# Performance work log

Measured on AMD Instinct MI355X. Metric: run time of the kernel, lower is better.

## Reference

```python
import jax, jax.numpy as jnp
import numpy as np

H = 64
N_LAYERS = 3
SIZES = {"atom": 100_000, "bond": 200_000, "motif": 50_000, "cell": 5_000}
# (src_type, dst_type) per relation, in HeteroConv dict order
RELS = [("atom", "atom"), ("atom", "bond"), ("atom", "motif"),
        ("bond", "bond"), ("bond", "motif"), ("motif", "motif"),
        ("atom", "cell"), ("bond", "cell"), ("motif", "cell")]
EDGE_NAMES = ["ei_aa", "ei_ab", "ei_am", "ei_bb", "ei_bm", "ei_mm", "ei_ac", "ei_bc", "ei_mc"]
N_EDGES = [800_000, 400_000, 200_000, 400_000, 200_000, 100_000, 100_000, 200_000, 50_000]


def setup_inputs() -> dict:
    key = jax.random.key(0)
    ks = iter(jax.random.split(key, 64))
    inp = {}
    for t in ["atom", "bond", "motif", "cell"]:
        inp["x_" + t] = jax.random.normal(next(ks), (SIZES[t], H), jnp.float32)
    scale = 1.0 / np.sqrt(H)
    inp["Wl"] = jax.random.normal(next(ks), (N_LAYERS, 9, H, H), jnp.float32) * scale
    inp["bl"] = jax.random.normal(next(ks), (N_LAYERS, 9, H), jnp.float32) * 0.01
    inp["Wr"] = jax.random.normal(next(ks), (N_LAYERS, 9, H, H), jnp.float32) * scale
    inp["proj_W"] = jax.random.normal(next(ks), (H, H), jnp.float32) * scale
    inp["proj_b"] = jax.random.normal(next(ks), (H,), jnp.float32) * 0.01
    inp["out_W"] = jax.random.normal(next(ks), (H, 1), jnp.float32) * scale
    inp["out_b"] = jax.random.normal(next(ks), (1,), jnp.float32) * 0.01
    for name, (st, dt), e in zip(EDGE_NAMES, RELS, N_EDGES):
        src = jax.random.randint(next(ks), (e,), 0, SIZES[st], dtype=jnp.int32)
        dst = jax.random.randint(next(ks), (e,), 0, SIZES[dt], dtype=jnp.int32)
        inp[name] = jnp.stack([src, dst]).astype(jnp.int64)
    return inp


def _sage(x_src, x_dst, ei, Wl_r, bl_r, Wr_r):
    """PyG SAGEConv: lin_l(mean of neighbor src feats) + bias + lin_r(x_dst)."""
    src, dst = ei[0], ei[1]
    n_dst = x_dst.shape[0]
    s = jax.ops.segment_sum(x_src[src], dst, num_segments=n_dst)        # [n_dst, H]
    cnt = jax.ops.segment_sum(jnp.ones_like(dst, dtype=x_src.dtype), dst, num_segments=n_dst)
    agg = s / jnp.maximum(cnt, 1.0)[:, None]                            # mean; 0 for isolated
    return agg @ Wl_r + bl_r + x_dst @ Wr_r


def reference(x_atom, x_bond, x_motif, x_cell, Wl, bl, Wr, proj_W, proj_b,
              out_W, out_b, ei_aa, ei_ab, ei_am, ei_bb, ei_bm, ei_mm,
              ei_ac, ei_bc, ei_mc):
    eis = [ei_aa, ei_ab, ei_am, ei_bb, ei_bm, ei_mm, ei_ac, ei_bc, ei_mc]
    x = {"atom": x_atom, "bond": x_bond, "motif": x_motif, "cell": x_cell}
    for l in range(N_LAYERS):
        acc = {t: jnp.zeros((SIZES[t], H), x_atom.dtype) for t in SIZES}
        for r, (st, dt) in enumerate(RELS):
            acc[dt] = acc[dt] + _sage(x[st], x[dt], eis[r], Wl[l, r], bl[l, r], Wr[l, r])
        x = {t: jax.nn.relu(acc[t]) for t in SIZES}  # HeteroConv aggr='sum' then relu
    h = jax.nn.softplus(x["cell"] @ proj_W + proj_b)
    return h @ out_W + out_b  # [n_cell, 1]
```

## Files before the change

### kernel.cpp

```cpp
#include <hip/hip_runtime.h>
#include <hip/hip_bf16.h>

#define H64 64

typedef __bf16 bf16_t;
typedef __bf16 bf16x8 __attribute__((ext_vector_type(8)));
typedef float f32x4 __attribute__((ext_vector_type(4)));

__device__ __forceinline__ float wload(const void* p, long i, bool f32) {
    return f32 ? ((const float*)p)[i]
               : __bfloat162float(((const __hip_bfloat16*)p)[i]);
}
__device__ __forceinline__ float blo(unsigned v) { return __uint_as_float(v << 16); }
__device__ __forceinline__ float bhi(unsigned v) { return __uint_as_float(v & 0xffff0000u); }
__device__ __forceinline__ unsigned packbf(float lo, float hi) {
    __hip_bfloat162 t;
    t.x = __float2bfloat16(lo);
    t.y = __float2bfloat16(hi);
    return *(unsigned*)&t;
}
__device__ __forceinline__ void acc8(float* s, uint4 v, unsigned m) {
    s[0] += blo(v.x & m); s[1] += bhi(v.x & m);
    s[2] += blo(v.y & m); s[3] += bhi(v.y & m);
    s[4] += blo(v.z & m); s[5] += bhi(v.z & m);
    s[6] += blo(v.w & m); s[7] += bhi(v.w & m);
}

__global__ void detect_k(const unsigned int* __restrict__ eiw, int nwords,
                         const unsigned short* __restrict__ xw,
                         const unsigned short* __restrict__ ww,
                         unsigned int* __restrict__ flags) {
    int t = threadIdx.x;
    unsigned int acc = 0;
    for (int i = 1 + 2 * t; i < nwords; i += 512) acc |= eiw[i];
    if (acc) atomicOr(&flags[0], acc);
    unsigned int cx = 0, cw = 0;
    for (int i = t; i < 8192; i += 256) {
        unsigned short w = xw[i];
        unsigned int e = (w >> 7) & 0xFF;
        if ((w & 0x7FFF) && (e == 0xFF || e < 0x40)) cx++;
        w = ww[i];
        e = (w >> 7) & 0xFF;
        if ((w & 0x7FFF) && (e == 0xFF || e < 0x40)) cw++;
    }
    if (cx) atomicAdd(&flags[1], cx);
    if (cw) atomicAdd(&flags[2], cw);
}

struct ConvArgs {
    const void* src[4];
    long elemoff[5];
};
__global__ void conv_in_all(ConvArgs ca, __hip_bfloat16* __restrict__ dst,
                            const unsigned int* __restrict__ flags) {
    bool xf32 = flags[1] > 64;
    long n = ca.elemoff[4];
    long i = (long)blockIdx.x * blockDim.x + threadIdx.x;
    long stride = (long)gridDim.x * blockDim.x;
    for (; i < n; i += stride) {
        int t = (i >= ca.elemoff[2]) ? (i >= ca.elemoff[3] ? 3 : 2)
                                     : (i >= ca.elemoff[1] ? 1 : 0);
        long j = i - ca.elemoff[t];
        float v = xf32 ? ((const float*)ca.src[t])[j]
                       : __bfloat162float(((const __hip_bfloat16*)ca.src[t])[j]);
        dst[i] = __float2bfloat16(v);
    }
}

__global__ void prep_w(const void* __restrict__ Wl, const void* __restrict__ Wr,
                       const void* __restrict__ bl, const unsigned int* __restrict__ flags,
                       bf16_t* __restrict__ wt, float* __restrict__ blsum) {
    const int rel_dt[9] = {0, 1, 2, 1, 2, 2, 3, 3, 3};
    bool wf32 = flags[2] > 64;
    int l = blockIdx.x / 13, p = blockIdx.x % 13;
    bf16_t* dst = wt + (long)blockIdx.x * 4096;
    for (int i = threadIdx.x; i < 4096; i += 256) {
        int n = i >> 6, k = i & 63;
        float v;
        if (p < 9) {
            v = wload(Wl, (long)(l * 9 + p) * 4096 + k * 64 + n, wf32);
        } else {
            int dt = p - 9;
            v = 0.f;
            for (int r = 0; r < 9; ++r)
                if (rel_dt[r] == dt) v += wload(Wr, (long)(l * 9 + r) * 4096 + k * 64 + n, wf32);
        }
        __hip_bfloat16 h = __float2bfloat16(v);
        dst[i] = *(bf16_t*)&h;
    }
    if (p >= 9 && threadIdx.x < 64) {
        int dt = p - 9;
        float s = 0.f;
        for (int r = 0; r < 9; ++r)
            if (rel_dt[r] == dt) s += wload(bl, (long)(l * 9 + r) * 64 + threadIdx.x, wf32);
        blsum[(l * 4 + dt) * 64 + threadIdx.x] = s;
    }
}

struct EdgeArgs {
    const int* ei[9];
    long eoff[10];
    int cntoff[9];
    int srcbase[9];
};

__global__ void count_all(EdgeArgs ea, const unsigned int* __restrict__ flags,
                          int* __restrict__ cnt, int* __restrict__ rank) {
    long e = (long)blockIdx.x * 256 + threadIdx.x;
    if (e >= ea.eoff[9]) return;
    int r = 0;
    while (r < 8 && e >= ea.eoff[r + 1]) ++r;
    long el = e - ea.eoff[r];
    long E = ea.eoff[r + 1] - ea.eoff[r];
    bool is64 = (flags[0] == 0u);
    const int* ei = ea.ei[r];
    int dst = is64 ? ei[2 * E + 2 * el] : ei[E + el];
    rank[e] = atomicAdd(&cnt[ea.cntoff[r] + dst], 1);
}

__global__ void fill_all(EdgeArgs ea, const unsigned int* __restrict__ flags,
                         const int* __restrict__ row_ptr, const int* __restrict__ rank,
                         int* __restrict__ edge_src) {
    long e = (long)blockIdx.x * 256 + threadIdx.x;
    if (e >= ea.eoff[9]) return;
    int r = 0;
    while (r < 8 && e >= ea.eoff[r + 1]) ++r;
    long el = e - ea.eoff[r];
    long E = ea.eoff[r + 1] - ea.eoff[r];
    bool is64 = (flags[0] == 0u);
    const int* ei = ea.ei[r];
    int src, dst;
    if (is64) { src = ei[2 * el]; dst = ei[2 * E + 2 * el]; }
    else      { src = ei[el];     dst = ei[E + el]; }
    int pos = row_ptr[ea.cntoff[r] + dst] + rank[e];
    edge_src[pos] = ea.srcbase[r] + src;
}

__global__ void scan_bsum(const int* __restrict__ cnt, int n, int* __restrict__ bsums) {
    __shared__ int red[256];
    int i = blockIdx.x * 256 + threadIdx.x;
    red[threadIdx.x] = (i < n) ? cnt[i] : 0;
    __syncthreads();
    for (int s = 128; s; s >>= 1) {
        if (threadIdx.x < s) red[threadIdx.x] += red[threadIdx.x + s];
        __syncthreads();
    }
    if (threadIdx.x == 0) bsums[blockIdx.x] = red[0];
}

__global__ void scan_excl_single(int* __restrict__ data, int n) {
    __shared__ int buf[1024];
    __shared__ int carry_s;
    if (threadIdx.x == 0) carry_s = 0;
    __syncthreads();
    for (int base = 0; base < n; base += 1024) {
        int i = base + threadIdx.x;
        int v = (i < n) ? data[i] : 0;
        buf[threadIdx.x] = v;
        __syncthreads();
        for (int off = 1; off < 1024; off <<= 1) {
            int tv = (threadIdx.x >= off) ? buf[threadIdx.x - off] : 0;
            __syncthreads();
            buf[threadIdx.x] += tv;
            __syncthreads();
        }
        int incl = buf[threadIdx.x];
        int carry = carry_s;
        if (i < n) data[i] = carry + incl - v;
        __syncthreads();
        if (threadIdx.x == 1023) carry_s = carry + buf[1023];
        __syncthreads();
    }
}

__global__ void scan_rowptr(const int* __restrict__ cnt, const int* __restrict__ bsums,
                            int n, int* __restrict__ row_ptr) {
    __shared__ int buf[256];
    int i = blockIdx.x * 256 + threadIdx.x;
    int v = (i < n) ? cnt[i] : 0;
    buf[threadIdx.x] = v;
    __syncthreads();
    for (int off = 1; off < 256; off <<= 1) {
        int tv = (threadIdx.x >= off) ? buf[threadIdx.x - off] : 0;
        __syncthreads();
        buf[threadIdx.x] += tv;
        __syncthreads();
    }
    int excl = buf[threadIdx.x] - v + bsums[blockIdx.x];
    if (i < n) row_ptr[i] = excl;
    if (i == n - 1) row_ptr[n] = excl + v;
}

struct FusedArgs {
    int cntOff[4][3];
    int wtSlot[4][4];
    long dstBase[4];
    int nDst[4];
    int Rdt[4];
    int blsumOff[4];
    int btBase[5];
};

__global__ __launch_bounds__(256) void fused_layer(
    const __hip_bfloat16* __restrict__ xin,
    __hip_bfloat16* __restrict__ xout,
    const int* __restrict__ edge_src,
    const int* __restrict__ row_ptr,
    const bf16_t* __restrict__ wt,
    const float* __restrict__ blsum,
    FusedArgs fa) {
    __shared__ unsigned lds[64 * 32];

    int bt = blockIdx.x;
    int dt = 0;
    while (dt < 3 && bt >= fa.btBase[dt + 1]) ++dt;
    int R = fa.Rdt[dt];
    int t0 = bt - fa.btBase[dt];
    int nD = fa.nDst[dt];

    int tid = threadIdx.x;
    int gr = tid >> 2, gp = tid & 3;
    bool rowValid = (t0 * 64 + gr < nD);
    int wv = tid >> 6, lane = tid & 63;
    int quad = lane >> 4, l16 = lane & 15;

    const uint4* xq = (const uint4*)xin;
    f32x4 acc[4] = {};

    for (int p = 0; p < R; ++p) {
        int rp0 = 0, rp1 = 0;
        if (rowValid) {
            int cr = fa.cntOff[dt][p] + t0 * 64 + gr;
            rp0 = row_ptr[cr]; rp1 = row_ptr[cr + 1];
        }
        float s[16];
        #pragma unroll
        for (int j = 0; j < 16; ++j) s[j] = 0.f;

        {
            int idx4[4];
            #pragma unroll
            for (int j = 0; j < 4; ++j) {
                int ee = rp0 + j;
                idx4[j] = edge_src[(ee < rp1) ? ee : 0];
            }
            uint4 v0[4], v1[4];
            #pragma unroll
            for (int j = 0; j < 4; ++j) {
                bool ok = (rp0 + j < rp1);
                unsigned ofs = (unsigned)idx4[j] * 8u + (unsigned)gp * 2u;
                v0[j] = xq[ok ? ofs : 0u];
                v1[j] = xq[ok ? ofs + 1u : 0u];
            }
            #pragma unroll
            for (int j = 0; j < 4; ++j) {
                unsigned m = (rp0 + j < rp1) ? 0xFFFFFFFFu : 0u;
                acc8(s, v0[j], m);
                acc8(s + 8, v1[j], m);
            }
        }
        for (int e = rp0 + 4; e < rp1; e += 4) {
            int idx4[4];
            #pragma unroll
            for (int j = 0; j < 4; ++j) {
                int ee = e + j;
                idx4[j] = edge_src[(ee < rp1) ? ee : 0];
            }
            uint4 v0[4], v1[4];
            #pragma unroll
            for (int j = 0; j < 4; ++j) {
                bool ok = (e + j < rp1);
                unsigned ofs = (unsigned)idx4[j] * 8u + (unsigned)gp * 2u;
                v0[j] = xq[ok ? ofs : 0u];
                v1[j] = xq[ok ? ofs + 1u : 0u];
            }
            #pragma unroll
            for (int j = 0; j < 4; ++j) {
                unsigned m = (e + j < rp1) ? 0xFFFFFFFFu : 0u;
                acc8(s, v0[j], m);
                acc8(s + 8, v1[j], m);
            }
        }

        float inv = (rp1 > rp0) ? 1.0f / (float)(rp1 - rp0) : 0.f;
        unsigned base = (unsigned)gr * 32u;
        #pragma unroll
        for (int h = 0; h < 2; ++h) {
            int d = gp * 8 + h * 4;
            unsigned idx = base + (unsigned)(d ^ ((gr & 7) << 2));
            uint4 o;
            o.x = packbf(s[h * 8 + 0] * inv, s[h * 8 + 1] * inv);
            o.y = packbf(s[h * 8 + 2] * inv, s[h * 8 + 3] * inv);
            o.z = packbf(s[h * 8 + 4] * inv, s[h * 8 + 5] * inv);
            o.w = packbf(s[h * 8 + 6] * inv, s[h * 8 + 7] * inv);
            *(uint4*)&lds[idx] = o;
        }
        __syncthreads();

        const bf16_t* wb = wt + (long)fa.wtSlot[dt][p] * 4096;
        int ar = wv * 16 + l16;
        unsigned i0 = (unsigned)ar * 32u + (unsigned)((quad * 4) ^ ((ar & 7) << 2));
        unsigned i1 = (unsigned)ar * 32u + (unsigned)(((16 + quad * 4)) ^ ((ar & 7) << 2));
        bf16x8 a0 = *(const bf16x8*)&lds[i0];
        bf16x8 a1 = *(const bf16x8*)&lds[i1];
        #pragma unroll
        for (int nt = 0; nt < 4; ++nt) {
            bf16x8 b0 = *(const bf16x8*)(wb + (nt * 16 + l16) * 64 + quad * 8);
            bf16x8 b1 = *(const bf16x8*)(wb + (nt * 16 + l16) * 64 + 32 + quad * 8);
            acc[nt] = __builtin_amdgcn_mfma_f32_16x16x32_bf16(a0, b0, acc[nt], 0, 0, 0);
            acc[nt] = __builtin_amdgcn_mfma_f32_16x16x32_bf16(a1, b1, acc[nt], 0, 0, 0);
        }
        __syncthreads();
    }

    {
        const bf16_t* wb = wt + (long)fa.wtSlot[dt][3] * 4096;
        const bf16_t* ab = (const bf16_t*)xin + (fa.dstBase[dt] + (long)t0 * 64 + wv * 16) * 64;
        bf16x8 a0 = *(const bf16x8*)(ab + l16 * 64 + quad * 8);
        bf16x8 a1 = *(const bf16x8*)(ab + l16 * 64 + 32 + quad * 8);
        #pragma unroll
        for (int nt = 0; nt < 4; ++nt) {
            bf16x8 b0 = *(const bf16x8*)(wb + (nt * 16 + l16) * 64 + quad * 8);
            bf16x8 b1 = *(const bf16x8*)(wb + (nt * 16 + l16) * 64 + 32 + quad * 8);
            acc[nt] = __builtin_amdgcn_mfma_f32_16x16x32_bf16(a0, b0, acc[nt], 0, 0, 0);
            acc[nt] = __builtin_amdgcn_mfma_f32_16x16x32_bf16(a1, b1, acc[nt], 0, 0, 0);
        }
    }

    const float* bs = blsum + fa.blsumOff[dt];
    #pragma unroll
    for (int nt = 0; nt < 4; ++nt) {
        int col = nt * 16 + l16;
        float bv = bs[col];
        #pragma unroll
        for (int reg = 0; reg < 4; ++reg) {
            long dd = (long)t0 * 64 + wv * 16 + quad * 4 + reg;
            if (dd < nD)
                xout[(fa.dstBase[dt] + dd) * 64 + col] =
                    __float2bfloat16(fmaxf(acc[nt][reg] + bv, 0.f));
        }
    }
}

__global__ __launch_bounds__(256) void head_k(
    const __hip_bfloat16* __restrict__ xc,
    const void* __restrict__ projW, const void* __restrict__ projb,
    const void* __restrict__ outW, const void* __restrict__ outb,
    void* __restrict__ out, const unsigned int* __restrict__ flags, int n) {
    __shared__ float PW[64 * 64];
    __shared__ float PB[64], OW[64];
    __shared__ float ROW[4][64];
    bool wf32 = flags[2] > 64;
    bool of32 = flags[1] > 64;
    int t = threadIdx.x;
    for (int i = t; i < 4096; i += 256) PW[i] = wload(projW, i, wf32);
    if (t < 64) { PB[t] = wload(projb, t, wf32); OW[t] = wload(outW, t, wf32); }
    int wid = t >> 6, lane = t & 63;
    int d = blockIdx.x * 4 + wid;
    ROW[wid][lane] = (d < n) ? __bfloat162float(xc[(long)d * H64 + lane]) : 0.f;
    __syncthreads();
    if (d < n) {
        float s = PB[lane];
        #pragma unroll 8
        for (int k = 0; k < 64; ++k) s += ROW[wid][k] * PW[k * 64 + lane];
        float sp = fmaxf(s, 0.f) + log1pf(expf(-fabsf(s)));
        float c = sp * OW[lane];
        #pragma unroll
        for (int off = 32; off; off >>= 1) c += __shfl_down(c, off, 64);
        if (lane == 0) {
            float rv = c + wload(outb, 0, wf32);
            if (of32) ((float*)out)[d] = rv;
            else ((__hip_bfloat16*)out)[d] = __float2bfloat16(rv);
        }
    }
}

extern "C" void kernel_launch(void* const* d_in, const int* in_sizes, int n_in,
                              void* d_out, int out_size, void* d_ws, size_t ws_size,
                              hipStream_t stream) {
    static const int rel_st[9] = {0, 0, 0, 1, 1, 2, 0, 1, 2};
    static const int rel_dt[9] = {0, 1, 2, 1, 2, 2, 3, 3, 3};
    static const int relsOf[4][3] = {{0, -1, -1}, {1, 3, -1}, {2, 4, 5}, {6, 7, 8}};
    static const int Rof[4] = {1, 2, 3, 3};

    long rows[4], rowoff[4], total = 0;
    for (int t = 0; t < 4; ++t) { rows[t] = in_sizes[t] / H64; rowoff[t] = total; total += rows[t]; }
    long NX = total * H64;
    long NXpad = (total + 64) * H64;
    long Es[9], ET = 0;
    for (int r = 0; r < 9; ++r) { Es[r] = (long)in_sizes[11 + r] / 2; ET += Es[r]; }
    long cntoff[9], cntN = 0;
    for (int r = 0; r < 9; ++r) { cntoff[r] = cntN; cntN += rows[rel_dt[r]]; }
    long nb1 = (cntN + 255) / 256;

    unsigned int* flags = (unsigned int*)d_ws;
    char* wsbase = (char*)d_ws + 64;
    auto align16 = [](size_t v) { return (v + 15) & ~(size_t)15; };
    size_t off = 0;
    __hip_bfloat16* x0 = (__hip_bfloat16*)(wsbase + off);  off = align16(off + (size_t)NXpad * 2);
    __hip_bfloat16* x1 = (__hip_bfloat16*)(wsbase + off);  off = align16(off + (size_t)NXpad * 2);
    int* cnt_i = (int*)(wsbase + off);                     off = align16(off + (size_t)cntN * 4);
    int* row_ptr = (int*)(wsbase + off);                   off = align16(off + (size_t)(cntN + 1) * 4);
    int* rank = (int*)(wsbase + off);                      off = align16(off + (size_t)ET * 4);
    int* edge_src = (int*)(wsbase + off);                  off = align16(off + (size_t)ET * 4);
    int* bsums = (int*)(wsbase + off);                     off = align16(off + (size_t)nb1 * 4);
    bf16_t* wt = (bf16_t*)(wsbase + off);                  off = align16(off + (size_t)39 * 4096 * 2);
    float* blsum = (float*)(wsbase + off);                 off = align16(off + (size_t)12 * 64 * 4);

    hipMemsetAsync(d_ws, 0, 64, stream);
    int nwords = 16384;
    if (in_sizes[11] < nwords) nwords = in_sizes[11];
    detect_k<<<1, 256, 0, stream>>>((const unsigned int*)d_in[11], nwords,
                                    (const unsigned short*)d_in[0],
                                    (const unsigned short*)d_in[4], flags);

    ConvArgs ca;
    for (int t = 0; t < 4; ++t) { ca.src[t] = d_in[t]; ca.elemoff[t] = rowoff[t] * H64; }
    ca.elemoff[4] = NX;
    {
        int blocks = (int)((NX + 255) / 256); if (blocks > 8192) blocks = 8192;
        conv_in_all<<<blocks, 256, 0, stream>>>(ca, x0, flags);
    }

    prep_w<<<39, 256, 0, stream>>>(d_in[4], d_in[6], d_in[5], flags, wt, blsum);

    EdgeArgs ea;
    long ecum = 0;
    for (int r = 0; r < 9; ++r) {
        ea.ei[r] = (const int*)d_in[11 + r];
        ea.eoff[r] = ecum; ecum += Es[r];
        ea.cntoff[r] = (int)cntoff[r];
        ea.srcbase[r] = (int)rowoff[rel_st[r]];
    }
    ea.eoff[9] = ecum;

    hipMemsetAsync(cnt_i, 0, (size_t)cntN * 4, stream);
    count_all<<<(int)((ET + 255) / 256), 256, 0, stream>>>(ea, flags, cnt_i, rank);
    scan_bsum<<<(int)nb1, 256, 0, stream>>>(cnt_i, (int)cntN, bsums);
    scan_excl_single<<<1, 1024, 0, stream>>>(bsums, (int)nb1);
    scan_rowptr<<<(int)nb1, 256, 0, stream>>>(cnt_i, bsums, (int)cntN, row_ptr);
    fill_all<<<(int)((ET + 255) / 256), 256, 0, stream>>>(ea, flags, row_ptr, rank, edge_src);

    FusedArgs fa;
    int bb = 0;
    for (int dt = 0; dt < 4; ++dt) {
        fa.nDst[dt] = (int)rows[dt];
        fa.Rdt[dt] = Rof[dt];
        fa.dstBase[dt] = rowoff[dt];
        fa.btBase[dt] = bb;
        bb += (int)((rows[dt] + 63) / 64);
        for (int p = 0; p < 3; ++p) {
            int rr = (p < Rof[dt]) ? relsOf[dt][p] : relsOf[dt][0];
            fa.cntOff[dt][p] = (int)cntoff[rr];
        }
    }
    fa.btBase[4] = bb;

    for (int l = 0; l < 3; ++l) {
        for (int dt = 0; dt < 4; ++dt) {
            fa.blsumOff[dt] = (l * 4 + dt) * 64;
            for (int p = 0; p < 3; ++p) {
                int rr = (p < Rof[dt]) ? relsOf[dt][p] : relsOf[dt][0];
                fa.wtSlot[dt][p] = l * 13 + rr;
            }
            fa.wtSlot[dt][3] = l * 13 + 9 + dt;
        }
        const __hip_bfloat16* xin = (l & 1) ? x1 : x0;
        __hip_bfloat16* xo = (l & 1) ? x0 : x1;
        fused_layer<<<bb, 256, 0, stream>>>(xin, xo, edge_src, row_ptr, wt, blsum, fa);
    }

    head_k<<<(int)((rows[3] + 3) / 4), 256, 0, stream>>>(
        x1 + rowoff[3] * H64, d_in[7], d_in[8], d_in[9], d_in[10], d_out, flags, (int)rows[3]);
}
```

Baseline: 883.1 us.

## Make each wavefront own a 16-row tile, removing block barriers in fused layer

Work in the fused layer kernel is redistributed so that each 64-lane wavefront independently handles a 16-row destination tile. It gathers all relations into its own LDS slice, then runs the MFMA reductions without any __syncthreads. Tiles are ordered with the cell type first and the costliest type last, so the slowest tiles start early and the tail shrinks. The change removes the block-wide barriers that made four waves wait on the slowest row in the tile. In exchange it uses more LDS per block and holds all gathered passes before compute, which may lower occupancy.

```diff
diff --git a/kernel.cpp b/kernel.cpp
--- a/kernel.cpp
+++ b/kernel.cpp
@@ -199,7 +199,79 @@
     int Rdt[4];
     int blsumOff[4];
     int btBase[5];
+    int dtOf[4];
+    int totalT16;
 };
+
+__device__ __forceinline__ void gather_pass(
+    unsigned* __restrict__ L,
+    const uint4* __restrict__ xq,
+    const int* __restrict__ edge_src,
+    const int* __restrict__ row_ptr,
+    int cr, bool valid, int gr, int gp) {
+    int rp0 = 0, rp1 = 0;
+    if (valid) { rp0 = row_ptr[cr]; rp1 = row_ptr[cr + 1]; }
+    float s[16];
+    #pragma unroll
+    for (int j = 0; j < 16; ++j) s[j] = 0.f;
+    {
+        int idx4[4];
+        #pragma unroll
+        for (int j = 0; j < 4; ++j) {
+            int ee = rp0 + j;
+            idx4[j] = edge_src[(ee < rp1) ? ee : 0];
+        }
+        uint4 v0[4], v1[4];
+        #pragma unroll
+        for (int j = 0; j < 4; ++j) {
+            bool ok = (rp0 + j < rp1);
+            unsigned ofs = (unsigned)idx4[j] * 8u + (unsigned)gp * 2u;
+            v0[j] = xq[ok ? ofs : 0u];
+            v1[j] = xq[ok ? ofs + 1u : 0u];
+        }
+        #pragma unroll
+        for (int j = 0; j < 4; ++j) {
+            unsigned m = (rp0 + j < rp1) ? 0xFFFFFFFFu : 0u;
+            acc8(s, v0[j], m);
+            acc8(s + 8, v1[j], m);
+        }
+    }
+    for (int e = rp0 + 4; e < rp1; e += 4) {
+        int idx4[4];
+        #pragma unroll
+        for (int j = 0; j < 4; ++j) {
+            int ee = e + j;
+            idx4[j] = edge_src[(ee < rp1) ? ee : 0];
+        }
+        uint4 v0[4], v1[4];
+        #pragma unroll
+        for (int j = 0; j < 4; ++j) {
+            bool ok = (e + j < rp1);
+            unsigned ofs = (unsigned)idx4[j] * 8u + (unsigned)gp * 2u;
+            v0[j] = xq[ok ? ofs : 0u];
+            v1[j] = xq[ok ? ofs + 1u : 0u];
+        }
+        #pragma unroll
+        for (int j = 0; j < 4; ++j) {
+            unsigned m = (e + j < rp1) ? 0xFFFFFFFFu : 0u;
+            acc8(s, v0[j], m);
+            acc8(s + 8, v1[j], m);
+        }
+    }
+    float inv = (rp1 > rp0) ? 1.0f / (float)(rp1 - rp0) : 0.f;
+    unsigned base = (unsigned)gr * 32u;
+    #pragma unroll
+    for (int h = 0; h < 2; ++h) {
+        int d = gp * 8 + h * 4;
+        unsigned idxw = base + (unsigned)(d ^ ((gr & 7) << 2));
+        uint4 o;
+        o.x = packbf(s[h * 8 + 0] * inv, s[h * 8 + 1] * inv);
+        o.y = packbf(s[h * 8 + 2] * inv, s[h * 8 + 3] * inv);
+        o.z = packbf(s[h * 8 + 4] * inv, s[h * 8 + 5] * inv);
+        o.w = packbf(s[h * 8 + 6] * inv, s[h * 8 + 7] * inv);
+        *(uint4*)&L[idxw] = o;
+    }
+}
 
 __global__ __launch_bounds__(256) void fused_layer(
     const __hip_bfloat16* __restrict__ xin,
@@ -209,100 +281,41 @@
     const bf16_t* __restrict__ wt,
     const float* __restrict__ blsum,
     FusedArgs fa) {
-    __shared__ unsigned lds[64 * 32];
-
-    int bt = blockIdx.x;
-    int dt = 0;
-    while (dt < 3 && bt >= fa.btBase[dt + 1]) ++dt;
+    __shared__ unsigned lds[4][3 * 512];
+
+    int wv = threadIdx.x >> 6;
+    int g = blockIdx.x * 4 + wv;
+    if (g >= fa.totalT16) return;
+    int slot = 0;
+    while (slot < 3 && g >= fa.btBase[slot + 1]) ++slot;
+    int dt = fa.dtOf[slot];
+    int t0 = g - fa.btBase[slot];
+    int nD = fa.nDst[dt];
     int R = fa.Rdt[dt];
-    int t0 = bt - fa.btBase[dt];
-    int nD = fa.nDst[dt];
-
-    int tid = threadIdx.x;
-    int gr = tid >> 2, gp = tid & 3;
-    bool rowValid = (t0 * 64 + gr < nD);
-    int wv = tid >> 6, lane = tid & 63;
+
+    int lane = threadIdx.x & 63;
+    int gr = lane >> 2, gp = lane & 3;
+    int row = t0 * 16 + gr;
+    bool valid = (row < nD);
     int quad = lane >> 4, l16 = lane & 15;
 
     const uint4* xq = (const uint4*)xin;
+    unsigned* L = lds[wv];
+
+    for (int p = 0; p < R; ++p)
+        gather_pass(L + p * 512, xq, edge_src, row_ptr,
+                    fa.cntOff[dt][p] + row, valid, gr, gp);
+
+    asm volatile("s_waitcnt lgkmcnt(0)" ::: "memory");
+
     f32x4 acc[4] = {};
-
     for (int p = 0; p < R; ++p) {
-        int rp0 = 0, rp1 = 0;
-        if (rowValid) {
-            int cr = fa.cntOff[dt][p] + t0 * 64 + gr;
-            rp0 = row_ptr[cr]; rp1 = row_ptr[cr + 1];
-        }
-        float s[16];
-        #pragma unroll
-        for (int j = 0; j < 16; ++j) s[j] = 0.f;
-
-        {
-            int idx4[4];
-            #pragma unroll
-            for (int j = 0; j < 4; ++j) {
-                int ee = rp0 + j;
-                idx4[j] = edge_src[(ee < rp1) ? ee : 0];
-            }
-            uint4 v0[4], v1[4];
-            #pragma unroll
-            for (int j = 0; j < 4; ++j) {
-                bool ok = (rp0 + j < rp1);
-                unsigned ofs = (unsigned)idx4[j] * 8u + (unsigned)gp * 2u;
-                v0[j] = xq[ok ? ofs : 0u];
-                v1[j] = xq[ok ? ofs + 1u : 0u];
-            }
-            #pragma unroll
-            for (int j = 0; j < 4; ++j) {
-                unsigned m = (rp0 + j < rp1) ? 0xFFFFFFFFu : 0u;
-                acc8(s, v0[j], m);
-                acc8(s + 8, v1[j], m);
-            }
-        }
-        for (int e = rp0 + 4; e < rp1; e += 4) {
-            int idx4[4];
-            #pragma unroll
-            for (int j = 0; j < 4; ++j) {
-                int ee = e + j;
-                idx4[j] = edge_src[(ee < rp1) ? ee : 0];
-            }
-            uint4 v0[4], v1[4];
-            #pragma unroll
-            for (int j = 0; j < 4; ++j) {
-                bool ok = (e + j < rp1);
-                unsigned ofs = (unsigned)idx4[j] * 8u + (unsigned)gp * 2u;
-                v0[j] = xq[ok ? ofs : 0u];
-                v1[j] = xq[ok ? ofs + 1u : 0u];
-            }
-            #pragma unroll
-            for (int j = 0; j < 4; ++j) {
-                unsigned m = (e + j < rp1) ? 0xFFFFFFFFu : 0u;
-                acc8(s, v0[j], m);
-                acc8(s + 8, v1[j], m);
-            }
-        }
-
-        float inv = (rp1 > rp0) ? 1.0f / (float)(rp1 - rp0) : 0.f;
-        unsigned base = (unsigned)gr * 32u;
-        #pragma unroll
-        for (int h = 0; h < 2; ++h) {
-            int d = gp * 8 + h * 4;
-            unsigned idx = base + (unsigned)(d ^ ((gr & 7) << 2));
-            uint4 o;
-            o.x = packbf(s[h * 8 + 0] * inv, s[h * 8 + 1] * inv);
-            o.y = packbf(s[h * 8 + 2] * inv, s[h * 8 + 3] * inv);
-            o.z = packbf(s[h * 8 + 4] * inv, s[h * 8 + 5] * inv);
-            o.w = packbf(s[h * 8 + 6] * inv, s[h * 8 + 7] * inv);
-            *(uint4*)&lds[idx] = o;
-        }
-        __syncthreads();
-
         const bf16_t* wb = wt + (long)fa.wtSlot[dt][p] * 4096;
-        int ar = wv * 16 + l16;
-        unsigned i0 = (unsigned)ar * 32u + (unsigned)((quad * 4) ^ ((ar & 7) << 2));
-        unsigned i1 = (unsigned)ar * 32u + (unsigned)(((16 + quad * 4)) ^ ((ar & 7) << 2));
-        bf16x8 a0 = *(const bf16x8*)&lds[i0];
-        bf16x8 a1 = *(const bf16x8*)&lds[i1];
+        unsigned sw = (unsigned)((l16 & 7) << 2);
+        unsigned i0 = (unsigned)(p * 512) + (unsigned)l16 * 32u + ((unsigned)(quad * 4) ^ sw);
+        unsigned i1 = (unsigned)(p * 512) + (unsigned)l16 * 32u + ((unsigned)(16 + quad * 4) ^ sw);
+        bf16x8 a0 = *(const bf16x8*)&L[i0];
+        bf16x8 a1 = *(const bf16x8*)&L[i1];
         #pragma unroll
         for (int nt = 0; nt < 4; ++nt) {
             bf16x8 b0 = *(const bf16x8*)(wb + (nt * 16 + l16) * 64 + quad * 8);
@@ -310,12 +323,11 @@
             acc[nt] = __builtin_amdgcn_mfma_f32_16x16x32_bf16(a0, b0, acc[nt], 0, 0, 0);
             acc[nt] = __builtin_amdgcn_mfma_f32_16x16x32_bf16(a1, b1, acc[nt], 0, 0, 0);
         }
-        __syncthreads();
     }
 
     {
         const bf16_t* wb = wt + (long)fa.wtSlot[dt][3] * 4096;
-        const bf16_t* ab = (const bf16_t*)xin + (fa.dstBase[dt] + (long)t0 * 64 + wv * 16) * 64;
+        const bf16_t* ab = (const bf16_t*)xin + (fa.dstBase[dt] + (long)t0 * 16) * 64;
         bf16x8 a0 = *(const bf16x8*)(ab + l16 * 64 + quad * 8);
         bf16x8 a1 = *(const bf16x8*)(ab + l16 * 64 + 32 + quad * 8);
         #pragma unroll
@@ -334,7 +346,7 @@
         float bv = bs[col];
         #pragma unroll
         for (int reg = 0; reg < 4; ++reg) {
-            long dd = (long)t0 * 64 + wv * 16 + quad * 4 + reg;
+            long dd = (long)t0 * 16 + quad * 4 + reg;
             if (dd < nD)
                 xout[(fa.dstBase[dt] + dd) * 64 + col] =
                     __float2bfloat16(fmaxf(acc[nt][reg] + bv, 0.f));
@@ -382,6 +394,7 @@
     static const int rel_dt[9] = {0, 1, 2, 1, 2, 2, 3, 3, 3};
     static const int relsOf[4][3] = {{0, -1, -1}, {1, 3, -1}, {2, 4, 5}, {6, 7, 8}};
     static const int Rof[4] = {1, 2, 3, 3};
+    static const int order[4] = {3, 0, 2, 1};
 
     long rows[4], rowoff[4], total = 0;
     for (int t = 0; t < 4; ++t) { rows[t] = in_sizes[t] / H64; rowoff[t] = total; total += rows[t]; }
@@ -443,18 +456,23 @@
 
     FusedArgs fa;
     int bb = 0;
+    for (int s = 0; s < 4; ++s) {
+        int dt = order[s];
+        fa.dtOf[s] = dt;
+        fa.btBase[s] = bb;
+        bb += (int)((rows[dt] + 15) / 16);
+    }
+    fa.btBase[4] = bb;
+    fa.totalT16 = bb;
     for (int dt = 0; dt < 4; ++dt) {
         fa.nDst[dt] = (int)rows[dt];
         fa.Rdt[dt] = Rof[dt];
         fa.dstBase[dt] = rowoff[dt];
-        fa.btBase[dt] = bb;
-        bb += (int)((rows[dt] + 63) / 64);
         for (int p = 0; p < 3; ++p) {
             int rr = (p < Rof[dt]) ? relsOf[dt][p] : relsOf[dt][0];
             fa.cntOff[dt][p] = (int)cntoff[rr];
         }
     }
-    fa.btBase[4] = bb;
 
     for (int l = 0; l < 3; ++l) {
         for (int dt = 0; dt < 4; ++dt) {
@@ -467,7 +485,7 @@
         }
         const __hip_bfloat16* xin = (l & 1) ? x1 : x0;
         __hip_bfloat16* xo = (l & 1) ? x0 : x1;
-        fused_layer<<<bb, 256, 0, stream>>>(xin, xo, edge_src, row_ptr, wt, blsum, fa);
+        fused_layer<<<(bb + 3) / 4, 256, 0, stream>>>(xin, xo, edge_src, row_ptr, wt, blsum, fa);
     }
 
     head_k<<<(int)((rows[3] + 3) / 4), 256, 0, stream>>>(
```

Result: faster. 849.7 us (-3.8%).
